# Optimization experiments

Measured on AMD Instinct MI355X. Metric: run time of the kernel, lower is better.

The kernel has to match this reference:

```python
import jax, jax.numpy as jnp
import numpy as np

N = 50000
E = 300000
D_IN = 128
H = 256
D_OUT = 256


def _glorot(key, shape):
    fan_in, fan_out = shape[0], shape[1]
    lim = float(np.sqrt(6.0 / (fan_in + fan_out)))
    return jax.random.uniform(key, shape, jnp.float32, -lim, lim)


def setup_inputs() -> dict:
    key = jax.random.key(0)
    ks = jax.random.split(key, 12)
    x = jax.random.normal(ks[0], (N, D_IN), jnp.float32)
    edge_index = jax.random.randint(ks[1], (2, E), 0, N, jnp.int64)
    return {
        "x": x,
        "edge_index": edge_index,
        "W1": _glorot(ks[2], (D_IN, H)),  "b1": jnp.zeros((H,), jnp.float32),
        "Wg1": _glorot(ks[3], (H, H)),    "bg1": jnp.zeros((H,), jnp.float32),
        "Wg2": _glorot(ks[4], (H, H)),    "bg2": jnp.zeros((H,), jnp.float32),
        "W2": _glorot(ks[5], (H, H)),     "b2": jnp.zeros((H,), jnp.float32),
        "W3": _glorot(ks[6], (H, D_OUT)), "b3": jnp.zeros((D_OUT,), jnp.float32),
    }


def _gcn_conv(h, src, dst, W, b):
    # PyG GCNConv: h' = D^-1/2 (A + I) D^-1/2 (h W) + b, deg counted at target with self-loops
    h = h @ W                                           # [N, H]
    deg = jnp.zeros((N,), h.dtype).at[dst].add(1.0) + 1.0
    dinv = jax.lax.rsqrt(deg)                           # deg^-1/2, [N]
    norm = dinv[src] * dinv[dst]                        # [E]
    msg = h[src] * norm[:, None]                        # gather + scale, [E, H]
    agg = jax.ops.segment_sum(msg, dst, num_segments=N)  # scatter-add
    agg = agg + h * (dinv * dinv)[:, None]              # self-loop contribution (norm = 1/deg)
    return agg + b


def reference(x, edge_index, W1, b1, Wg1, bg1, Wg2, bg2, W2, b2, W3, b3):
    src, dst = edge_index[0], edge_index[1]
    h = jax.nn.relu(x @ W1 + b1)
    h = jax.nn.relu(_gcn_conv(h, src, dst, Wg1, bg1))
    h = jax.nn.relu(_gcn_conv(h, src, dst, Wg2, bg2))
    h = jax.nn.relu(h @ W2 + b2)
    return jax.nn.softmax(h @ W3 + b3, axis=1)
```

## Files before the change

### kernel.cpp

```cpp
#include <hip/hip_runtime.h>
#include <math.h>

#define HDIM 256

typedef float floatx4 __attribute__((ext_vector_type(4)));
typedef __bf16 bf16x8 __attribute__((ext_vector_type(8)));
typedef unsigned short ushortx4 __attribute__((ext_vector_type(4)));

#define AS1C(p) ((const __attribute__((address_space(1))) void*)(p))
#define AS3(p)  ((__attribute__((address_space(3))) void*)(p))

__device__ inline unsigned short bf16_rn(float f) {
  unsigned u = __float_as_uint(f);
  return (unsigned short)((u + 0x7FFFu + ((u >> 16) & 1u)) >> 16);
}

__device__ inline void split_f32(float f, unsigned short& h, unsigned short& l) {
  unsigned short hb = bf16_rn(f);
  float hf = __uint_as_float(((unsigned)hb) << 16);
  h = hb;
  l = bf16_rn(f - hf);
}


__global__ __launch_bounds__(256)
void prep_w_staged(const float* __restrict__ W, unsigned short* __restrict__ SH,
                   unsigned short* __restrict__ SL, int K) {
  int idx = blockIdx.x * 256 + threadIdx.x;
  int total = K * 32;
  if (idx >= total) return;
  int chunksPerCb = total >> 1;
  int cb = (idx >= chunksPerCb) ? 1 : 0;
  int rem = idx - cb * chunksPerCb;
  int kt = rem >> 9;
  int chunk = rem & 511;
  int kc = chunk >> 7;
  int col = chunk & 127;
  const float* src = W + (size_t)(kt * 32 + kc * 8) * HDIM + cb * 128 + col;
#pragma unroll
  for (int e = 0; e < 8; ++e) {
    unsigned short h, l;
    split_f32(src[(size_t)e * HDIM], h, l);
    SH[(size_t)idx * 8 + e] = h;
    SL[(size_t)idx * 8 + e] = l;
  }
}


__global__ __launch_bounds__(256)
void deg_count_kernel(const int* __restrict__ ei, int* __restrict__ deg, int E) {
  int e = blockIdx.x * 256 + threadIdx.x;
  if (e < E) atomicAdd(&deg[ei[E + e]], 1);
}

__global__ __launch_bounds__(256)
void dinv_kernel(const int* __restrict__ deg, float* __restrict__ dinv, int n) {
  int i = blockIdx.x * 256 + threadIdx.x;
  if (i < n) dinv[i] = 1.0f / sqrtf((float)deg[i] + 1.0f);
}

__global__ __launch_bounds__(256)
void block_sum_kernel(const int* __restrict__ deg, int* __restrict__ bsum, int n) {
  __shared__ int sm[256];
  int t = threadIdx.x;
  int idx = blockIdx.x * 256 + t;
  sm[t] = (idx < n) ? deg[idx] : 0;
  __syncthreads();
  for (int off = 128; off > 0; off >>= 1) {
    if (t < off) sm[t] += sm[t + off];
    __syncthreads();
  }
  if (t == 0) bsum[blockIdx.x] = sm[0];
}

__global__ __launch_bounds__(256)
void scan_bsums_kernel(const int* __restrict__ bsum, int* __restrict__ boff,
                       int* __restrict__ rowptr, int nb, int n) {
  __shared__ int sm[256];
  int t = threadIdx.x;
  int v = (t < nb) ? bsum[t] : 0;
  sm[t] = v;
  __syncthreads();
  for (int off = 1; off < 256; off <<= 1) {
    int a = (t >= off) ? sm[t - off] : 0;
    __syncthreads();
    sm[t] += a;
    __syncthreads();
  }
  if (t < nb) boff[t] = sm[t] - v;
  if (t == 255) rowptr[n] = sm[255];
}

__global__ __launch_bounds__(256)
void scan_final_kernel(const int* __restrict__ deg, const int* __restrict__ boff,
                       int* __restrict__ rowptr, int* __restrict__ cursor, int n) {
  __shared__ int sm[256];
  int t = threadIdx.x;
  int idx = blockIdx.x * 256 + t;
  int v = (idx < n) ? deg[idx] : 0;
  sm[t] = v;
  __syncthreads();
  for (int off = 1; off < 256; off <<= 1) {
    int a = (t >= off) ? sm[t - off] : 0;
    __syncthreads();
    sm[t] += a;
    __syncthreads();
  }
  int excl = sm[t] - v + boff[blockIdx.x];
  if (idx < n) { rowptr[idx] = excl; cursor[idx] = excl; }
}

__global__ __launch_bounds__(256)
void fill_csr_kernel(const int* __restrict__ ei, int* __restrict__ cursor,
                     int* __restrict__ col, int E) {
  int e = blockIdx.x * 256 + threadIdx.x;
  if (e < E) {
    int s = ei[e];
    int d = ei[E + e];
    int p = atomicAdd(&cursor[d], 1);
    col[p] = s;
  }
}


template<bool BIAS, bool RELU>
__global__ __launch_bounds__(256, 3)
void mfma_gemm_splitA(const float* __restrict__ A,
                      const unsigned short* __restrict__ SWH,
                      const unsigned short* __restrict__ SWL,
                      const float* __restrict__ bias,
                      unsigned short* __restrict__ CH, unsigned short* __restrict__ CL,
                      int M, int K) {
  __shared__ __align__(16) unsigned short AsH[128 * 40];
  __shared__ __align__(16) unsigned short AsL[128 * 40];
  __shared__ __align__(16) unsigned short BsH[4096];
  __shared__ __align__(16) unsigned short BsL[4096];

  const int tid = threadIdx.x;
  const int w = tid >> 6;
  const int l = tid & 63;
  const int l15 = l & 15;
  const int quad = l >> 4;
  const int wm = w & 1;
  const int wn = w >> 1;
  const int bm = blockIdx.y * 128;
  const int bn = blockIdx.x * 128;
  const int ktc = K >> 5;

  floatx4 acc[4][4];
#pragma unroll
  for (int i = 0; i < 4; ++i)
#pragma unroll
    for (int j = 0; j < 4; ++j) acc[i][j] = (floatx4){0.f, 0.f, 0.f, 0.f};

  for (int kt = 0; kt < ktc; ++kt) {
    int k0 = kt * 32;
    float4 av[4];
#pragma unroll
    for (int i = 0; i < 4; ++i) {
      int chunk = i * 256 + tid;
      int row = chunk >> 3;
      int kc4 = chunk & 7;
      int grow = bm + row;
      if (grow > M - 1) grow = M - 1;
      av[i] = *(const float4*)(A + (size_t)grow * K + k0 + kc4 * 4);
    }

    __syncthreads();

    size_t wb = ((size_t)(blockIdx.x * ktc + kt)) * 4096;
#pragma unroll
    for (int j = 0; j < 2; ++j) {
      int c = j * 256 + tid;
      __builtin_amdgcn_global_load_lds(AS1C(SWH + wb + (size_t)c * 8),
                                       AS3(&BsH[(j * 256 + w * 64) * 8]), 16, 0, 0);
      __builtin_amdgcn_global_load_lds(AS1C(SWL + wb + (size_t)c * 8),
                                       AS3(&BsL[(j * 256 + w * 64) * 8]), 16, 0, 0);
    }

#pragma unroll
    for (int i = 0; i < 4; ++i) {
      int chunk = i * 256 + tid;
      int row = chunk >> 3;
      int kc4 = chunk & 7;
      unsigned short h0, h1, h2, h3, l0, l1, l2, l3;
      split_f32(av[i].x, h0, l0);
      split_f32(av[i].y, h1, l1);
      split_f32(av[i].z, h2, l2);
      split_f32(av[i].w, h3, l3);
      *(ushortx4*)&AsH[row * 40 + kc4 * 4] = (ushortx4){h0, h1, h2, h3};
      *(ushortx4*)&AsL[row * 40 + kc4 * 4] = (ushortx4){l0, l1, l2, l3};
    }

    __syncthreads();

    bf16x8 aH[4], aL[4];
#pragma unroll
    for (int fi = 0; fi < 4; ++fi) {
      int row = wm * 64 + fi * 16 + l15;
      aH[fi] = *(const bf16x8*)&AsH[row * 40 + quad * 8];
      aL[fi] = *(const bf16x8*)&AsL[row * 40 + quad * 8];
    }
#pragma unroll
    for (int fj = 0; fj < 4; ++fj) {
      int colL = wn * 64 + fj * 16 + l15;
      int cidx = quad * 128 + colL;
      bf16x8 bh = *(const bf16x8*)&BsH[cidx * 8];
      bf16x8 bl = *(const bf16x8*)&BsL[cidx * 8];
#pragma unroll
      for (int fi = 0; fi < 4; ++fi) {
        floatx4 t = acc[fi][fj];
        t = __builtin_amdgcn_mfma_f32_16x16x32_bf16(aH[fi], bl, t, 0, 0, 0);
        t = __builtin_amdgcn_mfma_f32_16x16x32_bf16(aL[fi], bh, t, 0, 0, 0);
        t = __builtin_amdgcn_mfma_f32_16x16x32_bf16(aH[fi], bh, t, 0, 0, 0);
        acc[fi][fj] = t;
      }
    }
  }

  float bcol[4];
#pragma unroll
  for (int fj = 0; fj < 4; ++fj)
    bcol[fj] = BIAS ? bias[bn + wn * 64 + fj * 16 + l15] : 0.f;

#pragma unroll
  for (int fi = 0; fi < 4; ++fi) {
    int rb = bm + wm * 64 + fi * 16 + quad * 4;
#pragma unroll
    for (int r = 0; r < 4; ++r) {
      int row = rb + r;
      if (row < M) {
        size_t base = (size_t)row * HDIM + bn + wn * 64 + l15;
#pragma unroll
        for (int fj = 0; fj < 4; ++fj) {
          float v = acc[fi][fj][r] + bcol[fj];
          if (RELU) v = fmaxf(v, 0.f);
          unsigned short h, lo;
          split_f32(v, h, lo);
          CH[base + fj * 16] = h;
          CL[base + fj * 16] = lo;
        }
      }
    }
  }
}


template<bool BIAS, bool RELU, bool SPLIT_OUT>
__global__ __launch_bounds__(256, 3)
void mfma_gemm_p(const unsigned short* __restrict__ AH, const unsigned short* __restrict__ AL,
                 const unsigned short* __restrict__ SWH, const unsigned short* __restrict__ SWL,
                 const float* __restrict__ bias,
                 float* __restrict__ C, unsigned short* __restrict__ CH,
                 unsigned short* __restrict__ CL, int M, int K) {
  __shared__ __align__(16) unsigned short AsH[4096];
  __shared__ __align__(16) unsigned short AsL[4096];
  __shared__ __align__(16) unsigned short BsH[4096];
  __shared__ __align__(16) unsigned short BsL[4096];

  const int tid = threadIdx.x;
  const int w = tid >> 6;
  const int l = tid & 63;
  const int l15 = l & 15;
  const int quad = l >> 4;
  const int wm = w & 1;
  const int wn = w >> 1;
  const int bm = blockIdx.y * 128;
  const int bn = blockIdx.x * 128;
  const int ktc = K >> 5;

  floatx4 acc[4][4];
#pragma unroll
  for (int i = 0; i < 4; ++i)
#pragma unroll
    for (int j = 0; j < 4; ++j) acc[i][j] = (floatx4){0.f, 0.f, 0.f, 0.f};

  for (int kt = 0; kt < ktc; ++kt) {
    __syncthreads();

#pragma unroll
    for (int i = 0; i < 2; ++i) {
      int L = i * 256 + tid;
      int row = L >> 2;
      int p = L & 3;
      int kc = p ^ (row & 3) ^ ((row >> 2) & 3);
      int grow = bm + row;
      if (grow > M - 1) grow = M - 1;
      const unsigned short* gH = AH + (size_t)grow * K + kt * 32 + kc * 8;
      const unsigned short* gL = AL + (size_t)grow * K + kt * 32 + kc * 8;
      __builtin_amdgcn_global_load_lds(AS1C(gH), AS3(&AsH[(i * 256 + w * 64) * 8]), 16, 0, 0);
      __builtin_amdgcn_global_load_lds(AS1C(gL), AS3(&AsL[(i * 256 + w * 64) * 8]), 16, 0, 0);
    }
    size_t wb = ((size_t)(blockIdx.x * ktc + kt)) * 4096;
#pragma unroll
    for (int j = 0; j < 2; ++j) {
      int c = j * 256 + tid;
      __builtin_amdgcn_global_load_lds(AS1C(SWH + wb + (size_t)c * 8),
                                       AS3(&BsH[(j * 256 + w * 64) * 8]), 16, 0, 0);
      __builtin_amdgcn_global_load_lds(AS1C(SWL + wb + (size_t)c * 8),
                                       AS3(&BsL[(j * 256 + w * 64) * 8]), 16, 0, 0);
    }

    __syncthreads();

    bf16x8 aH[4], aL[4];
#pragma unroll
    for (int fi = 0; fi < 4; ++fi) {
      int r = wm * 64 + fi * 16 + l15;
      int sw = quad ^ (r & 3) ^ ((r >> 2) & 3);
      aH[fi] = *(const bf16x8*)&AsH[(r * 4 + sw) * 8];
      aL[fi] = *(const bf16x8*)&AsL[(r * 4 + sw) * 8];
    }
#pragma unroll
    for (int fj = 0; fj < 4; ++fj) {
      int colL = wn * 64 + fj * 16 + l15;
      int cidx = quad * 128 + colL;
      bf16x8 bh = *(const bf16x8*)&BsH[cidx * 8];
      bf16x8 bl = *(const bf16x8*)&BsL[cidx * 8];
#pragma unroll
      for (int fi = 0; fi < 4; ++fi) {
        floatx4 t = acc[fi][fj];
        t = __builtin_amdgcn_mfma_f32_16x16x32_bf16(aH[fi], bl, t, 0, 0, 0);
        t = __builtin_amdgcn_mfma_f32_16x16x32_bf16(aL[fi], bh, t, 0, 0, 0);
        t = __builtin_amdgcn_mfma_f32_16x16x32_bf16(aH[fi], bh, t, 0, 0, 0);
        acc[fi][fj] = t;
      }
    }
  }

  float bcol[4];
#pragma unroll
  for (int fj = 0; fj < 4; ++fj)
    bcol[fj] = BIAS ? bias[bn + wn * 64 + fj * 16 + l15] : 0.f;

#pragma unroll
  for (int fi = 0; fi < 4; ++fi) {
    int rb = bm + wm * 64 + fi * 16 + quad * 4;
#pragma unroll
    for (int r = 0; r < 4; ++r) {
      int row = rb + r;
      if (row < M) {
        size_t base = (size_t)row * HDIM + bn + wn * 64 + l15;
        if (SPLIT_OUT) {
#pragma unroll
          for (int fj = 0; fj < 4; ++fj) {
            float v = acc[fi][fj][r] + bcol[fj];
            if (RELU) v = fmaxf(v, 0.f);
            unsigned short h, lo;
            split_f32(v, h, lo);
            CH[base + fj * 16] = h;
            CL[base + fj * 16] = lo;
          }
        } else {
#pragma unroll
          for (int fj = 0; fj < 4; ++fj) {
            float v = acc[fi][fj][r] + bcol[fj];
            if (RELU) v = fmaxf(v, 0.f);
            C[base + fj * 16] = v;
          }
        }
      }
    }
  }
}


__global__ __launch_bounds__(512, 4)
void mfma_gemm_softmax(const unsigned short* __restrict__ AH, const unsigned short* __restrict__ AL,
                       const unsigned short* __restrict__ SWH, const unsigned short* __restrict__ SWL,
                       const float* __restrict__ bias, float* __restrict__ out, int M, int K) {
  __shared__ __align__(16) unsigned short AsH[4096];
  __shared__ __align__(16) unsigned short AsL[4096];
  __shared__ __align__(16) unsigned short BsH[8192];
  __shared__ __align__(16) unsigned short BsL[8192];
  __shared__ float smax[128 * 4];
  __shared__ float ssum[128 * 4];

  const int tid = threadIdx.x;
  const int w = tid >> 6;
  const int l = tid & 63;
  const int l15 = l & 15;
  const int quad = l >> 4;
  const int wm = w & 1;
  const int wn = w >> 1;
  const int bm = blockIdx.x * 128;
  const int ktc = K >> 5;
  const int chunksPerCb = ktc * 512;

  floatx4 acc[4][4];
#pragma unroll
  for (int i = 0; i < 4; ++i)
#pragma unroll
    for (int j = 0; j < 4; ++j) acc[i][j] = (floatx4){0.f, 0.f, 0.f, 0.f};

  for (int kt = 0; kt < ktc; ++kt) {
    __syncthreads();

    {
      int L = tid;
      int row = L >> 2;
      int p = L & 3;
      int kc = p ^ (row & 3) ^ ((row >> 2) & 3);
      int grow = bm + row;
      if (grow > M - 1) grow = M - 1;
      const unsigned short* gH = AH + (size_t)grow * K + kt * 32 + kc * 8;
      const unsigned short* gL = AL + (size_t)grow * K + kt * 32 + kc * 8;
      __builtin_amdgcn_global_load_lds(AS1C(gH), AS3(&AsH[(w * 64) * 8]), 16, 0, 0);
      __builtin_amdgcn_global_load_lds(AS1C(gL), AS3(&AsL[(w * 64) * 8]), 16, 0, 0);
    }
#pragma unroll
    for (int j = 0; j < 2; ++j) {
      int pos = j * 512 + w * 64 + l;
      int kc = pos >> 8;
      int within = pos & 255;
      int cb = within >> 7;
      int colL = within & 127;
      size_t gi = (size_t)cb * chunksPerCb + (size_t)kt * 512 + kc * 128 + colL;
      __builtin_amdgcn_global_load_lds(AS1C(SWH + gi * 8),
                                       AS3(&BsH[(j * 512 + w * 64) * 8]), 16, 0, 0);
      __builtin_amdgcn_global_load_lds(AS1C(SWL + gi * 8),
                                       AS3(&BsL[(j * 512 + w * 64) * 8]), 16, 0, 0);
    }

    __syncthreads();

    bf16x8 aH[4], aL[4];
#pragma unroll
    for (int fi = 0; fi < 4; ++fi) {
      int r = wm * 64 + fi * 16 + l15;
      int sw = quad ^ (r & 3) ^ ((r >> 2) & 3);
      aH[fi] = *(const bf16x8*)&AsH[(r * 4 + sw) * 8];
      aL[fi] = *(const bf16x8*)&AsL[(r * 4 + sw) * 8];
    }
#pragma unroll
    for (int fj = 0; fj < 4; ++fj) {
      int colG = wn * 64 + fj * 16 + l15;
      int cidx = quad * 256 + colG;
      bf16x8 bh = *(const bf16x8*)&BsH[cidx * 8];
      bf16x8 bl = *(const bf16x8*)&BsL[cidx * 8];
#pragma unroll
      for (int fi = 0; fi < 4; ++fi) {
        floatx4 t = acc[fi][fj];
        t = __builtin_amdgcn_mfma_f32_16x16x32_bf16(aH[fi], bl, t, 0, 0, 0);
        t = __builtin_amdgcn_mfma_f32_16x16x32_bf16(aL[fi], bh, t, 0, 0, 0);
        t = __builtin_amdgcn_mfma_f32_16x16x32_bf16(aH[fi], bh, t, 0, 0, 0);
        acc[fi][fj] = t;
      }
    }
  }

  float bcol[4];
#pragma unroll
  for (int fj = 0; fj < 4; ++fj)
    bcol[fj] = bias[wn * 64 + fj * 16 + l15];

#pragma unroll
  for (int fi = 0; fi < 4; ++fi) {
#pragma unroll
    for (int r = 0; r < 4; ++r) {
      float mv = -3.4e38f;
#pragma unroll
      for (int fj = 0; fj < 4; ++fj) mv = fmaxf(mv, acc[fi][fj][r] + bcol[fj]);
#pragma unroll
      for (int off = 1; off < 16; off <<= 1) mv = fmaxf(mv, __shfl_xor(mv, off));
      int row = wm * 64 + fi * 16 + quad * 4 + r;
      if (l15 == 0) smax[row * 4 + wn] = mv;
    }
  }
  __syncthreads();

#pragma unroll
  for (int fi = 0; fi < 4; ++fi) {
#pragma unroll
    for (int r = 0; r < 4; ++r) {
      int row = wm * 64 + fi * 16 + quad * 4 + r;
      float gm = fmaxf(fmaxf(smax[row * 4 + 0], smax[row * 4 + 1]),
                       fmaxf(smax[row * 4 + 2], smax[row * 4 + 3]));
      float s = 0.f;
#pragma unroll
      for (int fj = 0; fj < 4; ++fj) {
        float p = expf(acc[fi][fj][r] + bcol[fj] - gm);
        acc[fi][fj][r] = p;
        s += p;
      }
#pragma unroll
      for (int off = 1; off < 16; off <<= 1) s += __shfl_xor(s, off);
      if (l15 == 0) ssum[row * 4 + wn] = s;
    }
  }
  __syncthreads();

#pragma unroll
  for (int fi = 0; fi < 4; ++fi) {
#pragma unroll
    for (int r = 0; r < 4; ++r) {
      int row = wm * 64 + fi * 16 + quad * 4 + r;
      int grow = bm + row;
      if (grow < M) {
        float inv = 1.0f / (ssum[row * 4 + 0] + ssum[row * 4 + 1] +
                            ssum[row * 4 + 2] + ssum[row * 4 + 3]);
        float* Cp = out + (size_t)grow * HDIM + wn * 64 + l15;
#pragma unroll
        for (int fj = 0; fj < 4; ++fj) Cp[fj * 16] = acc[fi][fj][r] * inv;
      }
    }
  }
}


__global__ __launch_bounds__(256)
void aggregate_b(const float* __restrict__ t, const float* __restrict__ dinv,
                 const int* __restrict__ rowptr, const int* __restrict__ col,
                 const float* __restrict__ bias,
                 unsigned short* __restrict__ OH, unsigned short* __restrict__ OL, int n) {
  int gw = (int)((blockIdx.x * 256 + threadIdx.x) >> 6);
  int lane = threadIdx.x & 63;
  if (gw >= n) return;
  float di = dinv[gw];
  float4 v = ((const float4*)(t + (size_t)gw * HDIM))[lane];
  float ss = di * di;
  float a0 = v.x * ss, a1 = v.y * ss, a2 = v.z * ss, a3 = v.w * ss;
  int e0 = rowptr[gw], e1 = rowptr[gw + 1];

  for (int base = e0; base < e1; base += 8) {
    int cs[8];
#pragma unroll
    for (int i = 0; i < 8; ++i) {
      int e = base + i;
      if (e > e1 - 1) e = e1 - 1;
      cs[i] = col[e];
    }
    float wg[8];
#pragma unroll
    for (int i = 0; i < 8; ++i)
      wg[i] = (base + i < e1) ? dinv[cs[i]] * di : 0.f;
    float4 rw[8];
#pragma unroll
    for (int i = 0; i < 8; ++i)
      rw[i] = ((const float4*)(t + (size_t)cs[i] * HDIM))[lane];
#pragma unroll
    for (int i = 0; i < 8; ++i) {
      a0 = fmaf(rw[i].x, wg[i], a0);
      a1 = fmaf(rw[i].y, wg[i], a1);
      a2 = fmaf(rw[i].z, wg[i], a2);
      a3 = fmaf(rw[i].w, wg[i], a3);
    }
  }

  float4 bb = ((const float4*)bias)[lane];
  float r0 = fmaxf(a0 + bb.x, 0.f);
  float r1 = fmaxf(a1 + bb.y, 0.f);
  float r2 = fmaxf(a2 + bb.z, 0.f);
  float r3 = fmaxf(a3 + bb.w, 0.f);
  unsigned short h0, h1, h2, h3, l0, l1, l2, l3;
  split_f32(r0, h0, l0);
  split_f32(r1, h1, l1);
  split_f32(r2, h2, l2);
  split_f32(r3, h3, l3);
  ((ushortx4*)(OH + (size_t)gw * HDIM))[lane] = (ushortx4){h0, h1, h2, h3};
  ((ushortx4*)(OL + (size_t)gw * HDIM))[lane] = (ushortx4){l0, l1, l2, l3};
}


extern "C" void kernel_launch(void* const* d_in, const int* in_sizes, int n_in,
                              void* d_out, int out_size, void* d_ws, size_t ws_size,
                              hipStream_t stream) {
  const float* x   = (const float*)d_in[0];
  const int*   ei  = (const int*)d_in[1];
  const float* W1  = (const float*)d_in[2];
  const float* b1  = (const float*)d_in[3];
  const float* Wg1 = (const float*)d_in[4];
  const float* bg1 = (const float*)d_in[5];
  const float* Wg2 = (const float*)d_in[6];
  const float* bg2 = (const float*)d_in[7];
  const float* W2  = (const float*)d_in[8];
  const float* b2  = (const float*)d_in[9];
  const float* W3  = (const float*)d_in[10];
  const float* b3  = (const float*)d_in[11];
  float* out = (float*)d_out;

  const int K1 = in_sizes[2] / HDIM;
  const int N  = in_sizes[0] / K1;
  const int E  = in_sizes[1] / 2;

  char* w = (char*)d_ws;
  auto alloc = [&](size_t bytes) -> char* {
    char* p = w;
    w += (bytes + 255) & ~(size_t)255;
    return p;
  };
  unsigned short* PH = (unsigned short*)alloc((size_t)N * HDIM * 2);
  unsigned short* PL = (unsigned short*)alloc((size_t)N * HDIM * 2);
  float* dinv   = (float*)alloc((size_t)N * sizeof(float));
  int*   deg    = (int*)alloc((size_t)N * sizeof(int));
  int*   rowptr = (int*)alloc((size_t)(N + 1) * sizeof(int));
  int*   cursor = (int*)alloc((size_t)N * sizeof(int));
  int*   col    = (int*)alloc((size_t)E * sizeof(int));
  const int nb  = (N + 255) / 256;
  int*   bsum   = (int*)alloc((size_t)nb * sizeof(int));
  int*   boff   = (int*)alloc((size_t)nb * sizeof(int));
  unsigned short* W1sH  = (unsigned short*)alloc((size_t)HDIM * K1 * 2);
  unsigned short* W1sL  = (unsigned short*)alloc((size_t)HDIM * K1 * 2);
  unsigned short* Wg1sH = (unsigned short*)alloc((size_t)HDIM * HDIM * 2);
  unsigned short* Wg1sL = (unsigned short*)alloc((size_t)HDIM * HDIM * 2);
  unsigned short* Wg2sH = (unsigned short*)alloc((size_t)HDIM * HDIM * 2);
  unsigned short* Wg2sL = (unsigned short*)alloc((size_t)HDIM * HDIM * 2);
  unsigned short* W2sH  = (unsigned short*)alloc((size_t)HDIM * HDIM * 2);
  unsigned short* W2sL  = (unsigned short*)alloc((size_t)HDIM * HDIM * 2);
  unsigned short* W3sH  = (unsigned short*)alloc((size_t)HDIM * HDIM * 2);
  unsigned short* W3sL  = (unsigned short*)alloc((size_t)HDIM * HDIM * 2);

  unsigned short* QH = (unsigned short*)out;
  unsigned short* QL = QH + (size_t)N * HDIM;

  const int ge = (E + 255) / 256;
  const int gn = (N + 255) / 256;

  prep_w_staged<<<(K1 * 32 + 255) / 256, 256, 0, stream>>>(W1, W1sH, W1sL, K1);
  prep_w_staged<<<(HDIM * 32 + 255) / 256, 256, 0, stream>>>(Wg1, Wg1sH, Wg1sL, HDIM);
  prep_w_staged<<<(HDIM * 32 + 255) / 256, 256, 0, stream>>>(Wg2, Wg2sH, Wg2sL, HDIM);
  prep_w_staged<<<(HDIM * 32 + 255) / 256, 256, 0, stream>>>(W2, W2sH, W2sL, HDIM);
  prep_w_staged<<<(HDIM * 32 + 255) / 256, 256, 0, stream>>>(W3, W3sH, W3sL, HDIM);

  hipMemsetAsync(deg, 0, (size_t)N * sizeof(int), stream);
  deg_count_kernel<<<ge, 256, 0, stream>>>(ei, deg, E);
  dinv_kernel<<<gn, 256, 0, stream>>>(deg, dinv, N);
  block_sum_kernel<<<nb, 256, 0, stream>>>(deg, bsum, N);
  scan_bsums_kernel<<<1, 256, 0, stream>>>(bsum, boff, rowptr, nb, N);
  scan_final_kernel<<<nb, 256, 0, stream>>>(deg, boff, rowptr, cursor, N);
  fill_csr_kernel<<<ge, 256, 0, stream>>>(ei, cursor, col, E);

  dim3 ggrid(2, (N + 127) / 128);
  const int gagg = (N + 3) / 4;
  const int gfuse = (N + 127) / 128;

  mfma_gemm_splitA<true, true><<<ggrid, 256, 0, stream>>>(x, W1sH, W1sL, b1, PH, PL, N, K1);
  mfma_gemm_p<false, false, false><<<ggrid, 256, 0, stream>>>(PH, PL, Wg1sH, Wg1sL, nullptr, out, nullptr, nullptr, N, HDIM);
  aggregate_b<<<gagg, 256, 0, stream>>>(out, dinv, rowptr, col, bg1, PH, PL, N);
  mfma_gemm_p<false, false, false><<<ggrid, 256, 0, stream>>>(PH, PL, Wg2sH, Wg2sL, nullptr, out, nullptr, nullptr, N, HDIM);
  aggregate_b<<<gagg, 256, 0, stream>>>(out, dinv, rowptr, col, bg2, PH, PL, N);
  mfma_gemm_p<true, true, true><<<ggrid, 256, 0, stream>>>(PH, PL, W2sH, W2sL, b2, nullptr, QH, QL, N, HDIM);
  mfma_gemm_softmax<<<gfuse, 512, 0, stream>>>(QH, QL, W3sH, W3sL, b3, out, N, HDIM);
}
```

Measured before the change: 419.1 us.

## Double-buffer GEMM LDS staging, pre-split input, and precompute per-edge source weights

The split-precision GEMM now double-buffers its A and B LDS tiles, issuing async loads for the next k-tile while MFMAs run on the current one. This drops one barrier per iteration and hides load latency, but doubles LDS use and lowers occupancy from 3 to 2 blocks per CU. The first-layer input is split into bf16 hi/lo planes by a separate kernel so the generic GEMM can replace the fused-split variant, which adds an extra pass over x. The CSR build also stores dinv[src] per edge, so aggregation reads weights sequentially instead of gathering dinv.

Result: slower. 433.2 us (+3.4%).

```diff
diff --git a/kernel.cpp b/kernel.cpp
--- a/kernel.cpp
+++ b/kernel.cpp
@@ -6,6 +6,7 @@
 typedef float floatx4 __attribute__((ext_vector_type(4)));
 typedef __bf16 bf16x8 __attribute__((ext_vector_type(8)));
 typedef unsigned short ushortx4 __attribute__((ext_vector_type(4)));
+typedef unsigned short ushortx8 __attribute__((ext_vector_type(8)));
 
 #define AS1C(p) ((const __attribute__((address_space(1))) void*)(p))
 #define AS3(p)  ((__attribute__((address_space(3))) void*)(p))
@@ -48,6 +49,28 @@
 
 
 __global__ __launch_bounds__(256)
+void split_plane(const float* __restrict__ in, unsigned short* __restrict__ H,
+                 unsigned short* __restrict__ L, int total8) {
+  int i = blockIdx.x * 256 + threadIdx.x;
+  if (i >= total8) return;
+  const float4* p = (const float4*)in;
+  float4 v0 = p[(size_t)i * 2];
+  float4 v1 = p[(size_t)i * 2 + 1];
+  float f[8] = {v0.x, v0.y, v0.z, v0.w, v1.x, v1.y, v1.z, v1.w};
+  ushortx8 hh, ll;
+#pragma unroll
+  for (int e = 0; e < 8; ++e) {
+    unsigned short h, l;
+    split_f32(f[e], h, l);
+    hh[e] = h;
+    ll[e] = l;
+  }
+  ((ushortx8*)H)[i] = hh;
+  ((ushortx8*)L)[i] = ll;
+}
+
+
+__global__ __launch_bounds__(256)
 void deg_count_kernel(const int* __restrict__ ei, int* __restrict__ deg, int E) {
   int e = blockIdx.x * 256 + threadIdx.x;
   if (e < E) atomicAdd(&deg[ei[E + e]], 1);
@@ -111,30 +134,31 @@
 }
 
 __global__ __launch_bounds__(256)
-void fill_csr_kernel(const int* __restrict__ ei, int* __restrict__ cursor,
-                     int* __restrict__ col, int E) {
+void fill_csr_kernel(const int* __restrict__ ei, const float* __restrict__ dinv,
+                     int* __restrict__ cursor, int* __restrict__ col,
+                     float* __restrict__ wsrc, int E) {
   int e = blockIdx.x * 256 + threadIdx.x;
   if (e < E) {
     int s = ei[e];
     int d = ei[E + e];
     int p = atomicAdd(&cursor[d], 1);
     col[p] = s;
-  }
-}
-
-
-template<bool BIAS, bool RELU>
-__global__ __launch_bounds__(256, 3)
-void mfma_gemm_splitA(const float* __restrict__ A,
-                      const unsigned short* __restrict__ SWH,
-                      const unsigned short* __restrict__ SWL,
-                      const float* __restrict__ bias,
-                      unsigned short* __restrict__ CH, unsigned short* __restrict__ CL,
-                      int M, int K) {
-  __shared__ __align__(16) unsigned short AsH[128 * 40];
-  __shared__ __align__(16) unsigned short AsL[128 * 40];
-  __shared__ __align__(16) unsigned short BsH[4096];
-  __shared__ __align__(16) unsigned short BsL[4096];
+    wsrc[p] = dinv[s];
+  }
+}
+
+
+template<bool BIAS, bool RELU, bool SPLIT_OUT>
+__global__ __launch_bounds__(256, 2)
+void mfma_gemm_p(const unsigned short* __restrict__ AH, const unsigned short* __restrict__ AL,
+                 const unsigned short* __restrict__ SWH, const unsigned short* __restrict__ SWL,
+                 const float* __restrict__ bias,
+                 float* __restrict__ C, unsigned short* __restrict__ CH,
+                 unsigned short* __restrict__ CL, int M, int K) {
+  __shared__ __align__(16) unsigned short AsH[2][4096];
+  __shared__ __align__(16) unsigned short AsL[2][4096];
+  __shared__ __align__(16) unsigned short BsH[2][4096];
+  __shared__ __align__(16) unsigned short BsL[2][4096];
 
   const int tid = threadIdx.x;
   const int w = tid >> 6;
@@ -153,131 +177,7 @@
 #pragma unroll
     for (int j = 0; j < 4; ++j) acc[i][j] = (floatx4){0.f, 0.f, 0.f, 0.f};
 
-  for (int kt = 0; kt < ktc; ++kt) {
-    int k0 = kt * 32;
-    float4 av[4];
-#pragma unroll
-    for (int i = 0; i < 4; ++i) {
-      int chunk = i * 256 + tid;
-      int row = chunk >> 3;
-      int kc4 = chunk & 7;
-      int grow = bm + row;
-      if (grow > M - 1) grow = M - 1;
-      av[i] = *(const float4*)(A + (size_t)grow * K + k0 + kc4 * 4);
-    }
-
-    __syncthreads();
-
-    size_t wb = ((size_t)(blockIdx.x * ktc + kt)) * 4096;
-#pragma unroll
-    for (int j = 0; j < 2; ++j) {
-      int c = j * 256 + tid;
-      __builtin_amdgcn_global_load_lds(AS1C(SWH + wb + (size_t)c * 8),
-                                       AS3(&BsH[(j * 256 + w * 64) * 8]), 16, 0, 0);
-      __builtin_amdgcn_global_load_lds(AS1C(SWL + wb + (size_t)c * 8),
-                                       AS3(&BsL[(j * 256 + w * 64) * 8]), 16, 0, 0);
-    }
-
-#pragma unroll
-    for (int i = 0; i < 4; ++i) {
-      int chunk = i * 256 + tid;
-      int row = chunk >> 3;
-      int kc4 = chunk & 7;
-      unsigned short h0, h1, h2, h3, l0, l1, l2, l3;
-      split_f32(av[i].x, h0, l0);
-      split_f32(av[i].y, h1, l1);
-      split_f32(av[i].z, h2, l2);
-      split_f32(av[i].w, h3, l3);
-      *(ushortx4*)&AsH[row * 40 + kc4 * 4] = (ushortx4){h0, h1, h2, h3};
-      *(ushortx4*)&AsL[row * 40 + kc4 * 4] = (ushortx4){l0, l1, l2, l3};
-    }
-
-    __syncthreads();
-
-    bf16x8 aH[4], aL[4];
-#pragma unroll
-    for (int fi = 0; fi < 4; ++fi) {
-      int row = wm * 64 + fi * 16 + l15;
-      aH[fi] = *(const bf16x8*)&AsH[row * 40 + quad * 8];
-      aL[fi] = *(const bf16x8*)&AsL[row * 40 + quad * 8];
-    }
-#pragma unroll
-    for (int fj = 0; fj < 4; ++fj) {
-      int colL = wn * 64 + fj * 16 + l15;
-      int cidx = quad * 128 + colL;
-      bf16x8 bh = *(const bf16x8*)&BsH[cidx * 8];
-      bf16x8 bl = *(const bf16x8*)&BsL[cidx * 8];
-#pragma unroll
-      for (int fi = 0; fi < 4; ++fi) {
-        floatx4 t = acc[fi][fj];
-        t = __builtin_amdgcn_mfma_f32_16x16x32_bf16(aH[fi], bl, t, 0, 0, 0);
-        t = __builtin_amdgcn_mfma_f32_16x16x32_bf16(aL[fi], bh, t, 0, 0, 0);
-        t = __builtin_amdgcn_mfma_f32_16x16x32_bf16(aH[fi], bh, t, 0, 0, 0);
-        acc[fi][fj] = t;
-      }
-    }
-  }
-
-  float bcol[4];
-#pragma unroll
-  for (int fj = 0; fj < 4; ++fj)
-    bcol[fj] = BIAS ? bias[bn + wn * 64 + fj * 16 + l15] : 0.f;
-
-#pragma unroll
-  for (int fi = 0; fi < 4; ++fi) {
-    int rb = bm + wm * 64 + fi * 16 + quad * 4;
-#pragma unroll
-    for (int r = 0; r < 4; ++r) {
-      int row = rb + r;
-      if (row < M) {
-        size_t base = (size_t)row * HDIM + bn + wn * 64 + l15;
-#pragma unroll
-        for (int fj = 0; fj < 4; ++fj) {
-          float v = acc[fi][fj][r] + bcol[fj];
-          if (RELU) v = fmaxf(v, 0.f);
-          unsigned short h, lo;
-          split_f32(v, h, lo);
-          CH[base + fj * 16] = h;
-          CL[base + fj * 16] = lo;
-        }
-      }
-    }
-  }
-}
-
-
-template<bool BIAS, bool RELU, bool SPLIT_OUT>
-__global__ __launch_bounds__(256, 3)
-void mfma_gemm_p(const unsigned short* __restrict__ AH, const unsigned short* __restrict__ AL,
-                 const unsigned short* __restrict__ SWH, const unsigned short* __restrict__ SWL,
-                 const float* __restrict__ bias,
-                 float* __restrict__ C, unsigned short* __restrict__ CH,
-                 unsigned short* __restrict__ CL, int M, int K) {
-  __shared__ __align__(16) unsigned short AsH[4096];
-  __shared__ __align__(16) unsigned short AsL[4096];
-  __shared__ __align__(16) unsigned short BsH[4096];
-  __shared__ __align__(16) unsigned short BsL[4096];
-
-  const int tid = threadIdx.x;
-  const int w = tid >> 6;
-  const int l = tid & 63;
-  const int l15 = l & 15;
-  const int quad = l >> 4;
-  const int wm = w & 1;
-  const int wn = w >> 1;
-  const int bm = blockIdx.y * 128;
-  const int bn = blockIdx.x * 128;
-  const int ktc = K >> 5;
-
-  floatx4 acc[4][4];
-#pragma unroll
-  for (int i = 0; i < 4; ++i)
-#pragma unroll
-    for (int j = 0; j < 4; ++j) acc[i][j] = (floatx4){0.f, 0.f, 0.f, 0.f};
-
-  for (int kt = 0; kt < ktc; ++kt) {
-    __syncthreads();
-
+  auto stage = [&](int kt, int buf) {
 #pragma unroll
     for (int i = 0; i < 2; ++i) {
       int L = i * 256 + tid;
@@ -288,35 +188,42 @@
       if (grow > M - 1) grow = M - 1;
       const unsigned short* gH = AH + (size_t)grow * K + kt * 32 + kc * 8;
       const unsigned short* gL = AL + (size_t)grow * K + kt * 32 + kc * 8;
-      __builtin_amdgcn_global_load_lds(AS1C(gH), AS3(&AsH[(i * 256 + w * 64) * 8]), 16, 0, 0);
-      __builtin_amdgcn_global_load_lds(AS1C(gL), AS3(&AsL[(i * 256 + w * 64) * 8]), 16, 0, 0);
+      __builtin_amdgcn_global_load_lds(AS1C(gH), AS3(&AsH[buf][(i * 256 + w * 64) * 8]), 16, 0, 0);
+      __builtin_amdgcn_global_load_lds(AS1C(gL), AS3(&AsL[buf][(i * 256 + w * 64) * 8]), 16, 0, 0);
     }
     size_t wb = ((size_t)(blockIdx.x * ktc + kt)) * 4096;
 #pragma unroll
     for (int j = 0; j < 2; ++j) {
       int c = j * 256 + tid;
       __builtin_amdgcn_global_load_lds(AS1C(SWH + wb + (size_t)c * 8),
-                                       AS3(&BsH[(j * 256 + w * 64) * 8]), 16, 0, 0);
+                                       AS3(&BsH[buf][(j * 256 + w * 64) * 8]), 16, 0, 0);
       __builtin_amdgcn_global_load_lds(AS1C(SWL + wb + (size_t)c * 8),
-                                       AS3(&BsL[(j * 256 + w * 64) * 8]), 16, 0, 0);
-    }
-
-    __syncthreads();
+                                       AS3(&BsL[buf][(j * 256 + w * 64) * 8]), 16, 0, 0);
+    }
+  };
+
+  stage(0, 0);
+  __syncthreads();
+  int cur = 0;
+
+#pragma unroll 1
+  for (int kt = 0; kt < ktc; ++kt) {
+    if (kt + 1 < ktc) stage(kt + 1, cur ^ 1);
 
     bf16x8 aH[4], aL[4];
 #pragma unroll
     for (int fi = 0; fi < 4; ++fi) {
       int r = wm * 64 + fi * 16 + l15;
       int sw = quad ^ (r & 3) ^ ((r >> 2) & 3);
-      aH[fi] = *(const bf16x8*)&AsH[(r * 4 + sw) * 8];
-      aL[fi] = *(const bf16x8*)&AsL[(r * 4 + sw) * 8];
+      aH[fi] = *(const bf16x8*)&AsH[cur][(r * 4 + sw) * 8];
+      aL[fi] = *(const bf16x8*)&AsL[cur][(r * 4 + sw) * 8];
     }
 #pragma unroll
     for (int fj = 0; fj < 4; ++fj) {
       int colL = wn * 64 + fj * 16 + l15;
       int cidx = quad * 128 + colL;
-      bf16x8 bh = *(const bf16x8*)&BsH[cidx * 8];
-      bf16x8 bl = *(const bf16x8*)&BsL[cidx * 8];
+      bf16x8 bh = *(const bf16x8*)&BsH[cur][cidx * 8];
+      bf16x8 bl = *(const bf16x8*)&BsL[cur][cidx * 8];
 #pragma unroll
       for (int fi = 0; fi < 4; ++fi) {
         floatx4 t = acc[fi][fj];
@@ -326,6 +233,9 @@
         acc[fi][fj] = t;
       }
     }
+
+    __syncthreads();
+    cur ^= 1;
   }
 
   float bcol[4];
@@ -511,7 +421,7 @@
 __global__ __launch_bounds__(256)
 void aggregate_b(const float* __restrict__ t, const float* __restrict__ dinv,
                  const int* __restrict__ rowptr, const int* __restrict__ col,
-                 const float* __restrict__ bias,
+                 const float* __restrict__ wsrc, const float* __restrict__ bias,
                  unsigned short* __restrict__ OH, unsigned short* __restrict__ OL, int n) {
   int gw = (int)((blockIdx.x * 256 + threadIdx.x) >> 6);
   int lane = threadIdx.x & 63;
@@ -524,16 +434,18 @@
 
   for (int base = e0; base < e1; base += 8) {
     int cs[8];
+    float wv[8];
 #pragma unroll
     for (int i = 0; i < 8; ++i) {
       int e = base + i;
       if (e > e1 - 1) e = e1 - 1;
       cs[i] = col[e];
+      wv[i] = wsrc[e];
     }
     float wg[8];
 #pragma unroll
     for (int i = 0; i < 8; ++i)
-      wg[i] = (base + i < e1) ? dinv[cs[i]] * di : 0.f;
+      wg[i] = (base + i < e1) ? wv[i] * di : 0.f;
     float4 rw[8];
 #pragma unroll
     for (int i = 0; i < 8; ++i)
@@ -596,6 +508,7 @@
   int*   rowptr = (int*)alloc((size_t)(N + 1) * sizeof(int));
   int*   cursor = (int*)alloc((size_t)N * sizeof(int));
   int*   col    = (int*)alloc((size_t)E * sizeof(int));
+  float* wcsr   = (float*)alloc((size_t)E * sizeof(float));
   const int nb  = (N + 255) / 256;
   int*   bsum   = (int*)alloc((size_t)nb * sizeof(int));
   int*   boff   = (int*)alloc((size_t)nb * sizeof(int));
@@ -610,6 +523,8 @@
   unsigned short* W3sH  = (unsigned short*)alloc((size_t)HDIM * HDIM * 2);
   unsigned short* W3sL  = (unsigned short*)alloc((size_t)HDIM * HDIM * 2);
 
+  unsigned short* XH = (unsigned short*)out;
+  unsigned short* XL = XH + (size_t)N * K1;
   unsigned short* QH = (unsigned short*)out;
   unsigned short* QL = QH + (size_t)N * HDIM;
 
@@ -628,17 +543,19 @@
   block_sum_kernel<<<nb, 256, 0, stream>>>(deg, bsum, N);
   scan_bsums_kernel<<<1, 256, 0, stream>>>(bsum, boff, rowptr, nb, N);
   scan_final_kernel<<<nb, 256, 0, stream>>>(deg, boff, rowptr, cursor, N);
-  fill_csr_kernel<<<ge, 256, 0, stream>>>(ei, cursor, col, E);
+  fill_csr_kernel<<<ge, 256, 0, stream>>>(ei, dinv, cursor, col, wcsr, E);
 
   dim3 ggrid(2, (N + 127) / 128);
   const int gagg = (N + 3) / 4;
   const int gfuse = (N + 127) / 128;
-
-  mfma_gemm_splitA<true, true><<<ggrid, 256, 0, stream>>>(x, W1sH, W1sL, b1, PH, PL, N, K1);
+  const int tot8 = N * K1 / 8;
+
+  split_plane<<<(tot8 + 255) / 256, 256, 0, stream>>>(x, XH, XL, tot8);
+  mfma_gemm_p<true, true, true><<<ggrid, 256, 0, stream>>>(XH, XL, W1sH, W1sL, b1, nullptr, PH, PL, N, K1);
   mfma_gemm_p<false, false, false><<<ggrid, 256, 0, stream>>>(PH, PL, Wg1sH, Wg1sL, nullptr, out, nullptr, nullptr, N, HDIM);
-  aggregate_b<<<gagg, 256, 0, stream>>>(out, dinv, rowptr, col, bg1, PH, PL, N);
+  aggregate_b<<<gagg, 256, 0, stream>>>(out, dinv, rowptr, col, wcsr, bg1, PH, PL, N);
   mfma_gemm_p<false, false, false><<<ggrid, 256, 0, stream>>>(PH, PL, Wg2sH, Wg2sL, nullptr, out, nullptr, nullptr, N, HDIM);
-  aggregate_b<<<gagg, 256, 0, stream>>>(out, dinv, rowptr, col, bg2, PH, PL, N);
+  aggregate_b<<<gagg, 256, 0, stream>>>(out, dinv, rowptr, col, wcsr, bg2, PH, PL, N);
   mfma_gemm_p<true, true, true><<<ggrid, 256, 0, stream>>>(PH, PL, W2sH, W2sL, b2, nullptr, QH, QL, N, HDIM);
   mfma_gemm_softmax<<<gfuse, 512, 0, stream>>>(QH, QL, W3sH, W3sL, b3, out, N, HDIM);
 }
```
